# Kernel tuning notes

Measured on AMD Instinct MI355X. Metric: run time of the kernel, lower is better.

Reference implementation:

```python
import jax, jax.numpy as jnp
import numpy as np

N_NODES = 50000
NUM_FEATURES = 128
HIDDEN = 128
OUT = 64
N_EDGES = 600000


def gcn_conv(x, edge_index, W, b, n_nodes):
    """PyG GCNConv: add self-loops, symmetric deg^{-1/2} normalization,
    x' = D^{-1/2}(A+I)D^{-1/2} (x @ W) + b."""
    xw = x @ W  # [N, out]
    loop = jnp.arange(n_nodes, dtype=edge_index.dtype)
    row = jnp.concatenate([edge_index[0], loop])  # source
    col = jnp.concatenate([edge_index[1], loop])  # target
    ones = jnp.ones(row.shape[0], dtype=xw.dtype)
    deg = jax.ops.segment_sum(ones, col, num_segments=n_nodes)  # in-degree incl. self-loop
    dis = jnp.where(deg > 0, jax.lax.rsqrt(deg), 0.0)
    norm = dis[row] * dis[col]  # [E+N]
    msg = xw[row] * norm[:, None]  # gather + scale
    agg = jax.ops.segment_sum(msg, col, num_segments=n_nodes)  # scatter-add
    return agg + b


def setup_inputs() -> dict:
    key = jax.random.key(0)
    ks = jax.random.split(key, 10)
    x = jax.random.normal(ks[0], (N_NODES, NUM_FEATURES), dtype=jnp.float32)
    edge_index = jax.random.randint(ks[1], (2, N_EDGES), 0, N_NODES, dtype=jnp.int64)
    s1 = 1.0 / np.sqrt(NUM_FEATURES)
    s2 = 1.0 / np.sqrt(HIDDEN)
    s3 = 1.0 / np.sqrt(OUT)
    # encoder GCN weights stored as [in, out]
    W_enc1 = jax.random.uniform(ks[2], (NUM_FEATURES, HIDDEN), jnp.float32, -s1, s1)
    b_enc1 = jnp.zeros((HIDDEN,), jnp.float32)
    W_enc2 = jax.random.uniform(ks[3], (HIDDEN, OUT), jnp.float32, -s2, s2)
    b_enc2 = jnp.zeros((OUT,), jnp.float32)
    # decoder Linear weights stored as [in, out]
    W_dec1 = jax.random.uniform(ks[4], (OUT, HIDDEN), jnp.float32, -s3, s3)
    b_dec1 = jax.random.uniform(ks[5], (HIDDEN,), jnp.float32, -s3, s3)
    W_dec2 = jax.random.uniform(ks[6], (HIDDEN, NUM_FEATURES), jnp.float32, -s2, s2)
    b_dec2 = jax.random.uniform(ks[7], (NUM_FEATURES,), jnp.float32, -s2, s2)
    return {"x": x, "edge_index": edge_index,
            "W_enc1": W_enc1, "b_enc1": b_enc1,
            "W_enc2": W_enc2, "b_enc2": b_enc2,
            "W_dec1": W_dec1, "b_dec1": b_dec1,
            "W_dec2": W_dec2, "b_dec2": b_dec2}


def reference(x, edge_index, W_enc1, b_enc1, W_enc2, b_enc2,
              W_dec1, b_dec1, W_dec2, b_dec2):
    n = x.shape[0]
    z = jax.nn.relu(gcn_conv(x, edge_index, W_enc1, b_enc1, n))
    z = jax.nn.relu(gcn_conv(z, edge_index, W_enc2, b_enc2, n))
    z = jax.nn.relu(z @ W_dec1 + b_dec1)
    x_hat = z @ W_dec2 + b_dec2
    return x_hat
```

## Files before the change

kernel.cpp:

```cpp
#include <hip/hip_runtime.h>
#include <hip/hip_bf16.h>


#define N_FEAT 128
#define HID    128
#define OUTD   64

typedef __hip_bfloat16 bf16;
typedef unsigned short u16;
typedef __attribute__((ext_vector_type(8))) short short8;
typedef __attribute__((ext_vector_type(4))) float f32x4;

__device__ __forceinline__ float bs2f(short s) {
    return __builtin_bit_cast(float, ((unsigned)(unsigned short)s) << 16);
}
__device__ __forceinline__ short f2bs(float f) {
    __hip_bfloat16 h = __float2bfloat16(f);
    return __builtin_bit_cast(short, h);
}


__global__ void k_prep(int* __restrict__ cnt, int n, int ZB,
                       const float* __restrict__ W1, const float* __restrict__ W2,
                       const float* __restrict__ Wd1, const float* __restrict__ Wd2,
                       bf16* __restrict__ W1t, bf16* __restrict__ W2t,
                       bf16* __restrict__ Wd1t, bf16* __restrict__ Wd2t) {
    int b = blockIdx.x;
    if (b < ZB) {
        int i4 = b * 256 + threadIdx.x;
        int n4 = n >> 2;
        if (i4 < n4) ((int4*)cnt)[i4] = make_int4(0, 0, 0, 0);
        if (i4 == 0) for (int i = n4 * 4; i < n; ++i) cnt[i] = 0;
        return;
    }
    int i = (b - ZB) * 256 + threadIdx.x;
    if (i < 16384) {
        int k = i >> 7, nn = i & 127;
        W1t[nn * 128 + k] = __float2bfloat16(W1[i]);
    } else if (i < 24576) {
        int j = i - 16384; int k = j >> 6, nn = j & 63;
        W2t[nn * 128 + k] = __float2bfloat16(W2[j]);
    } else if (i < 32768) {
        int j = i - 24576; int k = j >> 7, nn = j & 127;
        Wd1t[nn * 64 + k] = __float2bfloat16(Wd1[j]);
    } else if (i < 49152) {
        int j = i - 32768; int k = j >> 7, nn = j & 127;
        Wd2t[nn * 128 + k] = __float2bfloat16(Wd2[j]);
    }
}


__global__ void k_mega(const int* __restrict__ row, const int* __restrict__ col,
                       int E, int SL, int npg, int GB,
                       int* __restrict__ cnt, u16* __restrict__ slots, int n,
                       const float* __restrict__ x, const bf16* __restrict__ W1t,
                       bf16* __restrict__ xw1) {
    int b = blockIdx.x;
    if (b < GB) {
        if (b * 64 >= n) return;
        int t = threadIdx.x;
        int lane = t & 63, w = t >> 6;
        int quad = lane >> 4, l16 = lane & 15;
        int m0 = b * 64 + (w & 1) * 32;
        int nhw = (w >> 1) * 32;
        int kq = quad * 8;

        short8 zero8 = {0, 0, 0, 0, 0, 0, 0, 0};
        int mrow[2]; bool mok[2];
#pragma unroll
        for (int mi = 0; mi < 2; ++mi) {
            mrow[mi] = m0 + mi * 16 + l16;
            mok[mi] = mrow[mi] < n;
        }
        short8 af[2][4];
#pragma unroll
        for (int mi = 0; mi < 2; ++mi) {
#pragma unroll
            for (int kb = 0; kb < 4; ++kb) {
                if (!mok[mi]) { af[mi][kb] = zero8; continue; }
                const float* Af = x + (size_t)mrow[mi] * 128 + kb * 32 + kq;
                float4 a4 = *(const float4*)Af;
                float4 b4 = *(const float4*)(Af + 4);
                short8 r = {f2bs(a4.x), f2bs(a4.y), f2bs(a4.z), f2bs(a4.w),
                            f2bs(b4.x), f2bs(b4.y), f2bs(b4.z), f2bs(b4.w)};
                af[mi][kb] = r;
            }
        }
#pragma unroll
        for (int nc = 0; nc < 128; nc += 64) {
            int n0 = nc + nhw;
            f32x4 acc[2][2];
#pragma unroll
            for (int mi = 0; mi < 2; ++mi)
#pragma unroll
                for (int ni = 0; ni < 2; ++ni)
#pragma unroll
                    for (int r = 0; r < 4; ++r) acc[mi][ni][r] = 0.f;
#pragma unroll
            for (int kb = 0; kb < 4; ++kb) {
                short8 bfm[2];
#pragma unroll
                for (int ni = 0; ni < 2; ++ni) {
                    int nn = n0 + ni * 16 + l16;
                    bfm[ni] = *(const short8*)(W1t + (size_t)nn * 128 + kb * 32 + kq);
                }
#pragma unroll
                for (int mi = 0; mi < 2; ++mi)
#pragma unroll
                    for (int ni = 0; ni < 2; ++ni)
                        acc[mi][ni] = __builtin_amdgcn_mfma_f32_16x16x32_bf16(
                            af[mi][kb], bfm[ni], acc[mi][ni], 0, 0, 0);
            }
#pragma unroll
            for (int ni = 0; ni < 2; ++ni) {
                int nn = n0 + ni * 16 + l16;
#pragma unroll
                for (int mi = 0; mi < 2; ++mi)
#pragma unroll
                    for (int r = 0; r < 4; ++r) {
                        int m = m0 + mi * 16 + quad * 4 + r;
                        if (m < n)
                            ((short*)xw1)[(size_t)m * 128 + nn] = f2bs(acc[mi][ni][r]);
                    }
            }
        }
        return;
    }
    int bb = b - GB;
    int g = bb & 7;
    int s = bb >> 3;
    int lo = g * npg;
    int hi = lo + npg; if (hi > n) hi = n;
    int i4 = s * 256 + threadIdx.x;
    int E4 = E >> 2;
    if (i4 < E4) {
        int4 r4 = ((const int4*)row)[i4];
        int4 c4 = ((const int4*)col)[i4];
        int rr[4] = {r4.x, r4.y, r4.z, r4.w};
        int cc[4] = {c4.x, c4.y, c4.z, c4.w};
#pragma unroll
        for (int u = 0; u < 4; ++u) {
            int r = rr[u], c = cc[u];
            if (c >= lo && c < hi && (unsigned)r < (unsigned)n) {
                int pos = atomicAdd(&cnt[c], 1);
                if (pos < 64) slots[(size_t)c * 64 + pos] = (u16)r;
            }
        }
    }
    if (i4 == 0) {
        for (int e = E4 * 4; e < E; ++e) {
            int r = row[e], c = col[e];
            if (c >= lo && c < hi && (unsigned)r < (unsigned)n) {
                int pos = atomicAdd(&cnt[c], 1);
                if (pos < 64) slots[(size_t)c * 64 + pos] = (u16)r;
            }
        }
    }
}


__global__ void k_aggmm(const bf16* __restrict__ xw1, const int* __restrict__ cnt,
                        const u16* __restrict__ slots, const float* __restrict__ b1,
                        const bf16* __restrict__ W2t, bf16* __restrict__ xw2, int M) {
    __shared__ short h1s[64][136];
    int t = threadIdx.x;
    int lane = t & 63, w = t >> 6;
    int sub = lane >> 4, li = lane & 15;
    int blk = blockIdx.x;

    float4 c0 = *(const float4*)(b1 + li * 8);
    float4 c1 = *(const float4*)(b1 + li * 8 + 4);
    float bbv[8] = {c0.x, c0.y, c0.z, c0.w, c1.x, c1.y, c1.z, c1.w};

    for (int it = 0; it < 16; ++it) {
        int nd = blk * 64 + w * 16 + it;
        bool ok = nd < M;
        int craw = ok ? cnt[nd] : 0;
        int cn = ok ? min(craw, 64) + 1 : 0;
        const u16* sl = slots + (size_t)(ok ? nd : 0) * 64;

        float a[8] = {0.f, 0.f, 0.f, 0.f, 0.f, 0.f, 0.f, 0.f};
        for (int tt = sub; tt < cn; tt += 16) {
            bool va[4]; short8 v[4]; float ds[4];
#pragma unroll
            for (int u = 0; u < 4; ++u) {
                int ti = tt + u * 4;
                va[u] = ti < cn;
                int tc = va[u] ? ti : 0;
                int sI = (tc == cn - 1) ? nd : (int)sl[tc];
                v[u] = *((const short8*)(xw1 + (size_t)sI * 128) + li);
                ds[u] = rsqrtf((float)(cnt[sI] + 1));
            }
#pragma unroll
            for (int u = 0; u < 4; ++u)
                if (va[u]) {
#pragma unroll
                    for (int j = 0; j < 8; ++j) a[j] += ds[u] * bs2f(v[u][j]);
                }
        }
#pragma unroll
        for (int d = 32; d >= 16; d >>= 1)
#pragma unroll
            for (int j = 0; j < 8; ++j) a[j] += __shfl_down(a[j], d);

        if (lane < 16) {
            float dn = rsqrtf((float)(craw + 1));
            short8 o;
#pragma unroll
            for (int j = 0; j < 8; ++j) o[j] = f2bs(fmaxf(dn * a[j] + bbv[j], 0.f));
            *(short8*)&h1s[w * 16 + it][li * 8] = o;
        }
    }
    __syncthreads();

    int quad = lane >> 4, l16 = lane & 15;
    int m0 = (w & 1) * 32, nhw = (w >> 1) * 32, kq = quad * 8;

    short8 af[2][4];
#pragma unroll
    for (int mi = 0; mi < 2; ++mi)
#pragma unroll
        for (int kb = 0; kb < 4; ++kb)
            af[mi][kb] = *(const short8*)&h1s[m0 + mi * 16 + l16][kb * 32 + kq];

    f32x4 acc[2][2];
#pragma unroll
    for (int mi = 0; mi < 2; ++mi)
#pragma unroll
        for (int ni = 0; ni < 2; ++ni)
#pragma unroll
            for (int r = 0; r < 4; ++r) acc[mi][ni][r] = 0.f;
#pragma unroll
    for (int kb = 0; kb < 4; ++kb) {
        short8 bfm[2];
#pragma unroll
        for (int ni = 0; ni < 2; ++ni) {
            int nn = nhw + ni * 16 + l16;
            bfm[ni] = *(const short8*)(W2t + (size_t)nn * 128 + kb * 32 + kq);
        }
#pragma unroll
        for (int mi = 0; mi < 2; ++mi)
#pragma unroll
            for (int ni = 0; ni < 2; ++ni)
                acc[mi][ni] = __builtin_amdgcn_mfma_f32_16x16x32_bf16(
                    af[mi][kb], bfm[ni], acc[mi][ni], 0, 0, 0);
    }
#pragma unroll
    for (int ni = 0; ni < 2; ++ni) {
        int nn = nhw + ni * 16 + l16;
#pragma unroll
        for (int mi = 0; mi < 2; ++mi)
#pragma unroll
            for (int r = 0; r < 4; ++r) {
                int m = blk * 64 + m0 + mi * 16 + quad * 4 + r;
                if (m < M) {
                    float v = acc[mi][ni][r] * rsqrtf((float)(cnt[m] + 1));
                    ((short*)xw2)[(size_t)m * 64 + nn] = f2bs(v);
                }
            }
    }
}


__global__ void k_aggdec(const bf16* __restrict__ xw2, const int* __restrict__ cnt,
                         const u16* __restrict__ slots,
                         const float* __restrict__ b2,
                         const bf16* __restrict__ Wd1t, const float* __restrict__ bd1,
                         const bf16* __restrict__ Wd2t, const float* __restrict__ bd2,
                         float* __restrict__ out, int M) {
    __shared__ short h2s[64][72];
    __shared__ short h3s[64][136];
    int t = threadIdx.x;
    int lane = t & 63, w = t >> 6;
    int quad = lane >> 4, l16 = lane & 15;
    int blk = blockIdx.x;

    {
        int sub = lane >> 3;
        int li = lane & 7;
        int sgl = w * 8 + sub;
        int nd0 = blk * 64 + sgl;
        int nd1 = nd0 + 32;
        int cr0 = (nd0 < M) ? cnt[nd0] : -1;
        int cr1 = (nd1 < M) ? cnt[nd1] : -1;
        int cn0 = (nd0 < M) ? min(cr0, 64) + 1 : 0;
        int cn1 = (nd1 < M) ? min(cr1, 64) + 1 : 0;
        const u16* sl0 = slots + (size_t)min(nd0, M - 1) * 64;
        const u16* sl1 = slots + (size_t)min(nd1, M - 1) * 64;

        float a0[8] = {0.f, 0.f, 0.f, 0.f, 0.f, 0.f, 0.f, 0.f};
        float a1[8] = {0.f, 0.f, 0.f, 0.f, 0.f, 0.f, 0.f, 0.f};
        int tmax = cn0 > cn1 ? cn0 : cn1;
        for (int e = 0; e < tmax; e += 4) {
            bool va0[4], va1[4]; short8 v0[4], v1[4];
#pragma unroll
            for (int u = 0; u < 4; ++u) {
                int ei_ = e + u;
                va0[u] = ei_ < cn0;
                int t0 = va0[u] ? ei_ : 0;
                int s0 = (t0 == cn0 - 1) ? nd0 : (int)sl0[t0];
                v0[u] = *((const short8*)(xw2 + (size_t)s0 * 64) + li);
                va1[u] = ei_ < cn1;
                int t1 = va1[u] ? ei_ : 0;
                int s1 = (t1 == cn1 - 1) ? nd1 : (int)sl1[t1];
                v1[u] = *((const short8*)(xw2 + (size_t)s1 * 64) + li);
            }
#pragma unroll
            for (int u = 0; u < 4; ++u) {
                if (va0[u]) {
#pragma unroll
                    for (int j = 0; j < 8; ++j) a0[j] += bs2f(v0[u][j]);
                }
                if (va1[u]) {
#pragma unroll
                    for (int j = 0; j < 8; ++j) a1[j] += bs2f(v1[u][j]);
                }
            }
        }
        float dn0 = (nd0 < M) ? rsqrtf((float)(cr0 + 1)) : 0.f;
        float dn1 = (nd1 < M) ? rsqrtf((float)(cr1 + 1)) : 0.f;
        float4 c0 = *(const float4*)(b2 + li * 8);
        float4 c1 = *(const float4*)(b2 + li * 8 + 4);
        float bb[8] = {c0.x, c0.y, c0.z, c0.w, c1.x, c1.y, c1.z, c1.w};
        short8 o0, o1;
#pragma unroll
        for (int j = 0; j < 8; ++j) {
            o0[j] = f2bs(fmaxf(dn0 * a0[j] + bb[j], 0.f));
            o1[j] = f2bs(fmaxf(dn1 * a1[j] + bb[j], 0.f));
        }
        *(short8*)&h2s[sgl][li * 8] = o0;
        *(short8*)&h2s[sgl + 32][li * 8] = o1;
    }
    __syncthreads();

    int m0 = (w & 1) * 32;
    int nhw = (w >> 1) * 32;
    int kq = quad * 8;

    short8 af1[2][2];
#pragma unroll
    for (int mi = 0; mi < 2; ++mi)
#pragma unroll
        for (int kb = 0; kb < 2; ++kb)
            af1[mi][kb] = *(const short8*)&h2s[m0 + mi * 16 + l16][kb * 32 + kq];

#pragma unroll
    for (int nc = 0; nc < HID; nc += 64) {
        int n0 = nc + nhw;
        f32x4 acc[2][2];
#pragma unroll
        for (int mi = 0; mi < 2; ++mi)
#pragma unroll
            for (int ni = 0; ni < 2; ++ni)
#pragma unroll
                for (int r = 0; r < 4; ++r) acc[mi][ni][r] = 0.f;
#pragma unroll
        for (int kb = 0; kb < 2; ++kb) {
            short8 bfm[2];
#pragma unroll
            for (int ni = 0; ni < 2; ++ni) {
                int nn = n0 + ni * 16 + l16;
                bfm[ni] = *(const short8*)(Wd1t + (size_t)nn * OUTD + kb * 32 + kq);
            }
#pragma unroll
            for (int mi = 0; mi < 2; ++mi)
#pragma unroll
                for (int ni = 0; ni < 2; ++ni)
                    acc[mi][ni] = __builtin_amdgcn_mfma_f32_16x16x32_bf16(
                        af1[mi][kb], bfm[ni], acc[mi][ni], 0, 0, 0);
        }
#pragma unroll
        for (int ni = 0; ni < 2; ++ni) {
            int nn = n0 + ni * 16 + l16;
            float bv = bd1[nn];
#pragma unroll
            for (int mi = 0; mi < 2; ++mi)
#pragma unroll
                for (int r = 0; r < 4; ++r) {
                    int ml = m0 + mi * 16 + quad * 4 + r;
                    h3s[ml][nn] = f2bs(fmaxf(acc[mi][ni][r] + bv, 0.f));
                }
        }
    }
    __syncthreads();

    short8 af2[2][4];
#pragma unroll
    for (int mi = 0; mi < 2; ++mi)
#pragma unroll
        for (int kb = 0; kb < 4; ++kb)
            af2[mi][kb] = *(const short8*)&h3s[m0 + mi * 16 + l16][kb * 32 + kq];

#pragma unroll
    for (int nc = 0; nc < N_FEAT; nc += 64) {
        int n0 = nc + nhw;
        f32x4 acc[2][2];
#pragma unroll
        for (int mi = 0; mi < 2; ++mi)
#pragma unroll
            for (int ni = 0; ni < 2; ++ni)
#pragma unroll
                for (int r = 0; r < 4; ++r) acc[mi][ni][r] = 0.f;
#pragma unroll
        for (int kb = 0; kb < 4; ++kb) {
            short8 bfm[2];
#pragma unroll
            for (int ni = 0; ni < 2; ++ni) {
                int nn = n0 + ni * 16 + l16;
                bfm[ni] = *(const short8*)(Wd2t + (size_t)nn * HID + kb * 32 + kq);
            }
#pragma unroll
            for (int mi = 0; mi < 2; ++mi)
#pragma unroll
                for (int ni = 0; ni < 2; ++ni)
                    acc[mi][ni] = __builtin_amdgcn_mfma_f32_16x16x32_bf16(
                        af2[mi][kb], bfm[ni], acc[mi][ni], 0, 0, 0);
        }
#pragma unroll
        for (int ni = 0; ni < 2; ++ni) {
            int nn = n0 + ni * 16 + l16;
            float bv = bd2[nn];
#pragma unroll
            for (int mi = 0; mi < 2; ++mi)
#pragma unroll
                for (int r = 0; r < 4; ++r) {
                    int m = blk * 64 + m0 + mi * 16 + quad * 4 + r;
                    if (m < M)
                        out[(size_t)m * N_FEAT + nn] = acc[mi][ni][r] + bv;
                }
        }
    }
}


extern "C" void kernel_launch(void* const* d_in, const int* in_sizes, int n_in,
                              void* d_out, int out_size, void* d_ws, size_t ws_size,
                              hipStream_t stream) {
    const float* x   = (const float*)d_in[0];
    const int*   ei  = (const int*)d_in[1];
    const float* W1  = (const float*)d_in[2];
    const float* b1  = (const float*)d_in[3];
    const float* W2  = (const float*)d_in[4];
    const float* b2  = (const float*)d_in[5];
    const float* Wd1 = (const float*)d_in[6];
    const float* bd1 = (const float*)d_in[7];
    const float* Wd2 = (const float*)d_in[8];
    const float* bd2 = (const float*)d_in[9];

    const int n = in_sizes[0] / N_FEAT;
    const int E = in_sizes[1] / 2;
    const int* row = ei;
    const int* col = ei + E;

    char* wp = (char*)d_ws;
    bf16* xw1 = (bf16*)wp;  wp += (size_t)n * 128 * 2;
    bf16* xw2 = (bf16*)wp;  wp += (size_t)n * 64 * 2;
    bf16* W1t = (bf16*)wp;  wp += 128 * 128 * 2;
    bf16* W2t = (bf16*)wp;  wp += 128 * 64 * 2;
    bf16* Wd1t= (bf16*)wp;  wp += 64 * 128 * 2;
    bf16* Wd2t= (bf16*)wp;  wp += 128 * 128 * 2;
    int* cnt   = (int*)wp;   wp += (size_t)n * 4;
    u16* slots = (u16*)wp;   wp += (size_t)n * 64 * 2;

    int ZB = (n + 1023) / 1024;
    k_prep<<<ZB + 192, 256, 0, stream>>>(cnt, n, ZB, W1, W2, Wd1, Wd2,
                                         W1t, W2t, Wd1t, Wd2t);

    int E4 = E >> 2;
    int SL = (E4 + 255) / 256;
    int npg = (n + 7) / 8;
    int mg = (n + 63) / 64;
    int GB = (mg + 7) & ~7;
    k_mega<<<GB + 8 * SL, 256, 0, stream>>>(row, col, E, SL, npg, GB,
                                            cnt, slots, n, x, W1t, xw1);

    k_aggmm<<<mg, 256, 0, stream>>>(xw1, cnt, slots, b1, W2t, xw2, n);

    k_aggdec<<<mg, 256, 0, stream>>>(xw2, cnt, slots, b2,
                                     Wd1t, bd1, Wd2t, bd2, (float*)d_out, n);
}
```

Before: 213.1 us.

## Restructure layer-2 aggregation: stage neighbor lists in LDS, one node per quarter-wave, 512 threads

The aggregation+GEMM kernel now preloads each block's 64 neighbor slot lists, clamped counts and degree norms into shared memory up front. Each 16-lane group handles one whole node and walks its neighbors eight at a time, so the cross-subgroup shuffle reduction goes away. The block grows to 512 threads (8 waves), and the MFMA tile split gives each wave one 16-row tile. The aim is more memory-level parallelism on the gathers and fewer serialized global reads of cnt and slots. The trade-offs are extra LDS, a barrier, and load imbalance across nodes with different degrees inside a wave.

```diff
diff --git a/kernel.cpp b/kernel.cpp
--- a/kernel.cpp
+++ b/kernel.cpp
@@ -163,101 +163,104 @@
                         const u16* __restrict__ slots, const float* __restrict__ b1,
                         const bf16* __restrict__ W2t, bf16* __restrict__ xw2, int M) {
     __shared__ short h1s[64][136];
+    __shared__ u16 sl_s[64][72];
+    __shared__ float dn_s[64];
+    __shared__ int cn_s[64];
     int t = threadIdx.x;
     int lane = t & 63, w = t >> 6;
+    int blk = blockIdx.x;
+
+    if (t < 64) {
+        int nd = blk * 64 + t;
+        int craw = (nd < M) ? cnt[nd] : -1;
+        cn_s[t] = (nd < M) ? (min(craw, 64) + 1) : 0;
+        dn_s[t] = (nd < M) ? rsqrtf((float)(craw + 1)) : 0.f;
+    }
+    {
+        int node = t >> 3, chunk = t & 7;
+        int nd = blk * 64 + node;
+        int4 val = make_int4(0, 0, 0, 0);
+        if (nd < M)
+            val = ((const int4*)(slots + (size_t)nd * 64))[chunk];
+        *(int4*)&sl_s[node][chunk * 8] = val;
+    }
+    __syncthreads();
+
     int sub = lane >> 4, li = lane & 15;
-    int blk = blockIdx.x;
-
     float4 c0 = *(const float4*)(b1 + li * 8);
     float4 c1 = *(const float4*)(b1 + li * 8 + 4);
     float bbv[8] = {c0.x, c0.y, c0.z, c0.w, c1.x, c1.y, c1.z, c1.w};
 
-    for (int it = 0; it < 16; ++it) {
-        int nd = blk * 64 + w * 16 + it;
-        bool ok = nd < M;
-        int craw = ok ? cnt[nd] : 0;
-        int cn = ok ? min(craw, 64) + 1 : 0;
-        const u16* sl = slots + (size_t)(ok ? nd : 0) * 64;
-
+#pragma unroll
+    for (int rnd = 0; rnd < 2; ++rnd) {
+        int nl = w * 8 + rnd * 4 + sub;
+        int nd = blk * 64 + nl;
+        int cn = cn_s[nl];
         float a[8] = {0.f, 0.f, 0.f, 0.f, 0.f, 0.f, 0.f, 0.f};
-        for (int tt = sub; tt < cn; tt += 16) {
-            bool va[4]; short8 v[4]; float ds[4];
-#pragma unroll
-            for (int u = 0; u < 4; ++u) {
-                int ti = tt + u * 4;
+        for (int tt = 0; tt < cn; tt += 8) {
+            bool va[8]; short8 v[8]; float dsv[8];
+#pragma unroll
+            for (int u = 0; u < 8; ++u) {
+                int ti = tt + u;
                 va[u] = ti < cn;
                 int tc = va[u] ? ti : 0;
-                int sI = (tc == cn - 1) ? nd : (int)sl[tc];
+                int sI = (tc == cn - 1) ? nd : (int)sl_s[nl][tc];
                 v[u] = *((const short8*)(xw1 + (size_t)sI * 128) + li);
-                ds[u] = rsqrtf((float)(cnt[sI] + 1));
-            }
-#pragma unroll
-            for (int u = 0; u < 4; ++u)
+                dsv[u] = rsqrtf((float)(cnt[sI] + 1));
+            }
+#pragma unroll
+            for (int u = 0; u < 8; ++u)
                 if (va[u]) {
 #pragma unroll
-                    for (int j = 0; j < 8; ++j) a[j] += ds[u] * bs2f(v[u][j]);
-                }
-        }
-#pragma unroll
-        for (int d = 32; d >= 16; d >>= 1)
-#pragma unroll
-            for (int j = 0; j < 8; ++j) a[j] += __shfl_down(a[j], d);
-
-        if (lane < 16) {
-            float dn = rsqrtf((float)(craw + 1));
-            short8 o;
-#pragma unroll
-            for (int j = 0; j < 8; ++j) o[j] = f2bs(fmaxf(dn * a[j] + bbv[j], 0.f));
-            *(short8*)&h1s[w * 16 + it][li * 8] = o;
-        }
+                    for (int j = 0; j < 8; ++j) a[j] += dsv[u] * bs2f(v[u][j]);
+                }
+        }
+        float dn = dn_s[nl];
+        short8 o;
+#pragma unroll
+        for (int j = 0; j < 8; ++j) o[j] = f2bs(fmaxf(dn * a[j] + bbv[j], 0.f));
+        *(short8*)&h1s[nl][li * 8] = o;
     }
     __syncthreads();
 
     int quad = lane >> 4, l16 = lane & 15;
-    int m0 = (w & 1) * 32, nhw = (w >> 1) * 32, kq = quad * 8;
-
-    short8 af[2][4];
-#pragma unroll
-    for (int mi = 0; mi < 2; ++mi)
-#pragma unroll
-        for (int kb = 0; kb < 4; ++kb)
-            af[mi][kb] = *(const short8*)&h1s[m0 + mi * 16 + l16][kb * 32 + kq];
-
-    f32x4 acc[2][2];
-#pragma unroll
-    for (int mi = 0; mi < 2; ++mi)
-#pragma unroll
-        for (int ni = 0; ni < 2; ++ni)
-#pragma unroll
-            for (int r = 0; r < 4; ++r) acc[mi][ni][r] = 0.f;
+    int mt = w & 3;
+    int nh = w >> 2;
+    int kq = quad * 8;
+
+    short8 af[4];
+#pragma unroll
+    for (int kb = 0; kb < 4; ++kb)
+        af[kb] = *(const short8*)&h1s[mt * 16 + l16][kb * 32 + kq];
+
+    f32x4 acc[2];
+#pragma unroll
+    for (int ni = 0; ni < 2; ++ni)
+#pragma unroll
+        for (int r = 0; r < 4; ++r) acc[ni][r] = 0.f;
 #pragma unroll
     for (int kb = 0; kb < 4; ++kb) {
         short8 bfm[2];
 #pragma unroll
         for (int ni = 0; ni < 2; ++ni) {
-            int nn = nhw + ni * 16 + l16;
+            int nn = nh * 32 + ni * 16 + l16;
             bfm[ni] = *(const short8*)(W2t + (size_t)nn * 128 + kb * 32 + kq);
         }
 #pragma unroll
-        for (int mi = 0; mi < 2; ++mi)
-#pragma unroll
-            for (int ni = 0; ni < 2; ++ni)
-                acc[mi][ni] = __builtin_amdgcn_mfma_f32_16x16x32_bf16(
-                    af[mi][kb], bfm[ni], acc[mi][ni], 0, 0, 0);
+        for (int ni = 0; ni < 2; ++ni)
+            acc[ni] = __builtin_amdgcn_mfma_f32_16x16x32_bf16(
+                af[kb], bfm[ni], acc[ni], 0, 0, 0);
     }
 #pragma unroll
     for (int ni = 0; ni < 2; ++ni) {
-        int nn = nhw + ni * 16 + l16;
-#pragma unroll
-        for (int mi = 0; mi < 2; ++mi)
-#pragma unroll
-            for (int r = 0; r < 4; ++r) {
-                int m = blk * 64 + m0 + mi * 16 + quad * 4 + r;
-                if (m < M) {
-                    float v = acc[mi][ni][r] * rsqrtf((float)(cnt[m] + 1));
-                    ((short*)xw2)[(size_t)m * 64 + nn] = f2bs(v);
-                }
-            }
+        int nn = nh * 32 + ni * 16 + l16;
+#pragma unroll
+        for (int r = 0; r < 4; ++r) {
+            int ml = mt * 16 + quad * 4 + r;
+            int m = blk * 64 + ml;
+            if (m < M)
+                ((short*)xw2)[(size_t)m * 64 + nn] = f2bs(acc[ni][r] * dn_s[ml]);
+        }
     }
 }
 
@@ -474,7 +477,7 @@
     k_mega<<<GB + 8 * SL, 256, 0, stream>>>(row, col, E, SL, npg, GB,
                                             cnt, slots, n, x, W1t, xw1);
 
-    k_aggmm<<<mg, 256, 0, stream>>>(xw1, cnt, slots, b1, W2t, xw2, n);
+    k_aggmm<<<mg, 512, 0, stream>>>(xw1, cnt, slots, b1, W2t, xw2, n);
 
     k_aggdec<<<mg, 256, 0, stream>>>(xw2, cnt, slots, b2,
                                      Wd1t, bd1, Wd2t, bd2, (float*)d_out, n);
```

After: 190.9 us. -10.4%, faster.
